# Performance work log

Hardware: AMD Instinct MI355X
Metric: run time of the kernel (lower is better)

Reference implementation:

```python
import jax, jax.numpy as jnp
import numpy as np

D_MODEL = 5120
NUM_HEADS = 128
HEAD_DIM = D_MODEL // NUM_HEADS  # 40
LATENT = 1536


def setup_inputs() -> dict:
    key = jax.random.key(0)
    ks = jax.random.split(key, 9)
    B, S = 2, 1024
    scale = 0.02
    return {
        "x": jax.random.normal(ks[0], (B, S, D_MODEL), dtype=jnp.float32),
        "Wq": jax.random.normal(ks[1], (D_MODEL, D_MODEL), dtype=jnp.float32) * scale,
        "bq": jnp.zeros((D_MODEL,), dtype=jnp.float32),
        "Wc": jax.random.normal(ks[2], (D_MODEL, LATENT), dtype=jnp.float32) * scale,
        "bc": jnp.zeros((LATENT,), dtype=jnp.float32),
        "Wk": jax.random.normal(ks[3], (LATENT, D_MODEL), dtype=jnp.float32) * scale,
        "bk": jnp.zeros((D_MODEL,), dtype=jnp.float32),
        "Wv": jax.random.normal(ks[4], (LATENT, D_MODEL), dtype=jnp.float32) * scale,
        "bv": jnp.zeros((D_MODEL,), dtype=jnp.float32),
    }


def reference(x, Wq, bq, Wc, bc, Wk, bk, Wv, bv):
    B, S, _ = x.shape
    H, Dh = NUM_HEADS, HEAD_DIM
    # projections
    q = x @ Wq + bq                     # [B,S,D]
    kv_latent = x @ Wc + bc             # [B,S,L]
    k = kv_latent @ Wk + bk             # [B,S,D]
    v = kv_latent @ Wv + bv             # [B,S,D]
    # split heads -> [B,H,S,Dh]
    q = q.reshape(B, S, H, Dh).transpose(0, 2, 1, 3)
    k = k.reshape(B, S, H, Dh).transpose(0, 2, 1, 3)
    v = v.reshape(B, S, H, Dh).transpose(0, 2, 1, 3)
    scores = jnp.einsum("bhqd,bhkd->bhqk", q, k) / jnp.sqrt(jnp.float32(Dh))
    attn = jax.nn.softmax(scores, axis=-1)
    out = jnp.einsum("bhqk,bhkd->bhqd", attn, v)  # [B,H,S,Dh]
    return out.transpose(0, 2, 1, 3).reshape(B, S, H * Dh)
```

## Files before the change

### kernel.cpp

```cpp
#include <hip/hip_runtime.h>
#include <hip/hip_bf16.h>

typedef __attribute__((ext_vector_type(8))) __bf16 bf16x8;
typedef __attribute__((ext_vector_type(4))) __bf16 bf16x4;
typedef __attribute__((ext_vector_type(4))) float f32x4;

#define MFMA16(a, b, c) __builtin_amdgcn_mfma_f32_16x16x32_bf16((a), (b), (c), 0, 0, 0)

#if __has_builtin(__builtin_amdgcn_exp2f)
#define EXP2F(x) __builtin_amdgcn_exp2f(x)
#else
#define EXP2F(x) exp2f(x)
#endif

#define GLDS16(g, l)                                                             \
    __builtin_amdgcn_global_load_lds((const __attribute__((address_space(1))) void*)(g), \
                                     (__attribute__((address_space(3))) void*)(l), 16, 0, 0)

#define BARRIER()                          \
    do {                                   \
        asm volatile("" ::: "memory");     \
        __builtin_amdgcn_s_barrier();      \
        asm volatile("" ::: "memory");     \
    } while (0)

#define WAIT_LGKM0() asm volatile("s_waitcnt lgkmcnt(0)" ::: "memory")
#define VM6 asm volatile("s_waitcnt vmcnt(6)" ::: "memory")
#define VM8 asm volatile("s_waitcnt vmcnt(8)" ::: "memory")
#define VM0 asm volatile("s_waitcnt vmcnt(0)" ::: "memory")
#define VMNONE ((void)0)
#define KEEP(x) x
#define DROP(x)

static __device__ __forceinline__ unsigned short cvt_bf(float f) {
    return __builtin_bit_cast(unsigned short, (__bf16)f);
}

static __device__ __forceinline__ bf16x8 bf8_zero() {
    uint4 z = make_uint4(0, 0, 0, 0);
    return __builtin_bit_cast(bf16x8, z);
}

__global__ __launch_bounds__(256) void xconv(const float* __restrict__ X,
                                             unsigned short* __restrict__ Xb, int n) {
    int i = (blockIdx.x * 256 + threadIdx.x) * 4;
    if (i < n) {
        float4 f = *(const float4*)(X + i);
        ushort4 o;
        o.x = cvt_bf(f.x); o.y = cvt_bf(f.y); o.z = cvt_bf(f.z); o.w = cvt_bf(f.w);
        *(ushort4*)(Xb + i) = o;
    }
}

__global__ __launch_bounds__(256) void wconv(const float* __restrict__ W,
                                             unsigned short* __restrict__ WT, int K, int N) {
    __shared__ unsigned short tile[32][33];
    int n0 = blockIdx.x * 32, k0 = blockIdx.y * 32;
    int c = threadIdx.x & 31, r8 = threadIdx.x >> 5;
#pragma unroll
    for (int it = 0; it < 4; ++it) {
        int r = r8 + it * 8;
        tile[r][c] = cvt_bf(W[(size_t)(k0 + r) * N + n0 + c]);
    }
    __syncthreads();
    int k2 = (threadIdx.x & 15) * 2, n8 = threadIdx.x >> 4;
#pragma unroll
    for (int it = 0; it < 2; ++it) {
        int n = n8 + it * 16;
        ushort2 o;
        o.x = tile[k2][n];
        o.y = tile[k2 + 1][n];
        *(ushort2*)&WT[(size_t)(n0 + n) * K + k0 + k2] = o;
    }
}


#define STAGE_A(S, H, KT)                                                              \
    do {                                                                               \
        GLDS16(aS[H][0] + (size_t)(KT) * 64, &Abuf[S][(H) * 8192 + wid * 512]);        \
        GLDS16(aS[H][1] + (size_t)(KT) * 64, &Abuf[S][(H) * 8192 + 4096 + wid * 512]); \
    } while (0)
#define STAGE_B(S, H, KT)                                                              \
    do {                                                                               \
        GLDS16(bS[H][0] + (size_t)(KT) * 64, &Bbuf[S][(H) * 8192 + wid * 512]);        \
        GLDS16(bS[H][1] + (size_t)(KT) * 64, &Bbuf[S][(H) * 8192 + 4096 + wid * 512]); \
    } while (0)

#define LDA_HALF(S, QM)                                                                   \
    do {                                                                                  \
        _Pragma("unroll") for (int mi = 0; mi < 4; ++mi)                                  \
            _Pragma("unroll") for (int kh = 0; kh < 2; ++kh)                              \
                af[mi][kh] =                                                              \
                    *(const bf16x8*)&Abuf[S][((QM) * 8192 + aoff + mi * 1024) ^ (kh * 32)]; \
    } while (0)
#define LDB_HALF(S, QN, BF)                                                               \
    do {                                                                                  \
        _Pragma("unroll") for (int ni = 0; ni < 2; ++ni)                                  \
            _Pragma("unroll") for (int kh = 0; kh < 2; ++kh)                              \
                BF[ni][kh] =                                                              \
                    *(const bf16x8*)&Bbuf[S][((QN) * 8192 + boff + ni * 1024) ^ (kh * 32)]; \
    } while (0)

#define MMAQ(QM, QN, BF)                                                                \
    do {                                                                                \
        _Pragma("unroll") for (int mi = 0; mi < 4; ++mi)                                \
            _Pragma("unroll") for (int ni = 0; ni < 2; ++ni)                            \
                _Pragma("unroll") for (int kh = 0; kh < 2; ++kh)                        \
                    acc[(QM) * 4 + mi][(QN) * 2 + ni] =                                 \
                        MFMA16(af[mi][kh], BF[ni][kh], acc[(QM) * 4 + mi][(QN) * 2 + ni]); \
    } while (0)

#define KTILE_V2(S, T, STG1, STG2, VMOP, RDNEXT)       \
    {                                                  \
        const int s_ = (S);                            \
        LDB_HALF(s_, 1, bf1);                          \
        STG1(STAGE_B(s_ ^ 1, 0, (T) + 1);)             \
        __builtin_amdgcn_s_setprio(1);                 \
        MMAQ(0, 0, bf0);                               \
        __builtin_amdgcn_s_setprio(0);                 \
        WAIT_LGKM0();                                  \
        BARRIER();                                     \
        STG2(STAGE_A(s_, 0, (T) + 2);                  \
             STAGE_B(s_, 1, (T) + 2);)                 \
        __builtin_amdgcn_s_setprio(1);                 \
        MMAQ(0, 1, bf1);                               \
        __builtin_amdgcn_s_setprio(0);                 \
        LDA_HALF(s_, 1);                               \
        __builtin_amdgcn_s_setprio(1);                 \
        MMAQ(1, 1, bf1);                               \
        __builtin_amdgcn_s_setprio(0);                 \
        WAIT_LGKM0();                                  \
        BARRIER();                                     \
        STG2(STAGE_A(s_, 1, (T) + 2);)                 \
        __builtin_amdgcn_s_setprio(1);                 \
        MMAQ(1, 0, bf0);                               \
        __builtin_amdgcn_s_setprio(0);                 \
        VMOP;                                          \
        BARRIER();                                     \
        RDNEXT(LDA_HALF(s_ ^ 1, 0); LDB_HALF(s_ ^ 1, 0, bf0);) \
    }

__global__ __launch_bounds__(512, 2) void gemm256(const unsigned short* __restrict__ A, int lda,
                                                  const unsigned short* __restrict__ BT, int ldb,
                                                  const float* __restrict__ bias0,
                                                  const float* __restrict__ bias1, int nsplit,
                                                  unsigned short* __restrict__ C, int ldc,
                                                  int K, float s0, float s1, int gx) {
    __shared__ __align__(16) unsigned short Abuf[2][16384];
    __shared__ __align__(16) unsigned short Bbuf[2][16384];

    int nwg = gridDim.x, orig = blockIdx.x;
    int cpx = nwg >> 3;
    int wgid = (orig & 7) * cpx + (orig >> 3);
    int tm = wgid / gx, tn = wgid % gx;
    int m0 = tm * 256, n0 = tn * 256;

    int tid = threadIdx.x, lane = tid & 63, wid = tid >> 6;
    int wm = wid >> 2, wn = wid & 3;
    int lrow = lane & 15, lkg = lane >> 4;

    int t5 = tid >> 3;
    int cole = ((tid & 7) ^ ((tid >> 3) & 7)) << 3;
    const unsigned short* aS[2][2];
    const unsigned short* bS[2][2];
#pragma unroll
    for (int H = 0; H < 2; ++H)
#pragma unroll
        for (int c = 0; c < 2; ++c) {
            int rA = (c << 7) | (H << 6) | t5;
            int rB = (((c << 1) | (t5 >> 5)) << 6) | (H << 5) | (t5 & 31);
            aS[H][c] = A + (size_t)(m0 + rA) * lda + cole;
            bS[H][c] = BT + (size_t)(n0 + rB) * ldb + cole;
        }

    int xorc = (lkg * 8) ^ ((lrow & 7) << 3);
    int aoff = wm * 4096 + lrow * 64 + xorc;
    int boff = wn * 2048 + lrow * 64 + xorc;

    f32x4 acc[8][4];
#pragma unroll
    for (int i = 0; i < 8; ++i)
#pragma unroll
        for (int j = 0; j < 4; ++j) acc[i][j] = (f32x4){0.f, 0.f, 0.f, 0.f};
    bf16x8 af[4][2], bf0[2][2], bf1[2][2];

    const int nkt = K >> 6;

    STAGE_A(0, 0, 0); STAGE_A(0, 1, 0); STAGE_B(0, 0, 0); STAGE_B(0, 1, 0);
    STAGE_A(1, 0, 1); STAGE_B(1, 1, 1); STAGE_A(1, 1, 1);
    VM6;
    BARRIER();
    LDA_HALF(0, 0);
    LDB_HALF(0, 0, bf0);

    int t = 0;
    for (; t + 2 < nkt; ++t) KTILE_V2(t & 1, t, KEEP, KEEP, VM6, KEEP);
    KTILE_V2(t & 1, t, KEEP, DROP, VM0, KEEP);
    ++t;
    KTILE_V2(t & 1, t, DROP, DROP, VMNONE, DROP);

#pragma unroll
    for (int ni = 0; ni < 4; ++ni) {
        int col = n0 + wn * 64 + ni * 16 + lrow;
        float bval = (col < nsplit) ? bias0[col] : bias1[col - nsplit];
        float scl = (col < nsplit) ? s0 : s1;
#pragma unroll
        for (int mi = 0; mi < 8; ++mi) {
            int row = m0 + wm * 128 + mi * 16 + lkg * 4;
#pragma unroll
            for (int j = 0; j < 4; ++j)
                C[(size_t)(row + j) * ldc + col] = cvt_bf((acc[mi][ni][j] + bval) * scl);
        }
    }
}

#define STG128(S, KT)                                                                  \
    do {                                                                               \
        _Pragma("unroll") for (int i_ = 0; i_ < 4; ++i_)                               \
            GLDS16(Ag + (size_t)(i_ * 32) * lda + (size_t)(KT) * 64,                   \
                   &Abuf[S][i_ * 2048 + wid * 512]);                                   \
        _Pragma("unroll") for (int i_ = 0; i_ < 4; ++i_)                               \
            GLDS16(Bg + (size_t)(i_ * 32) * ldb + (size_t)(KT) * 64,                   \
                   &Bbuf[S][i_ * 2048 + wid * 512]);                                   \
    } while (0)

__global__ __launch_bounds__(256, 2) void gemm128(const unsigned short* __restrict__ A, int lda,
                                                  const unsigned short* __restrict__ BT, int ldb,
                                                  const float* __restrict__ bias0,
                                                  const float* __restrict__ bias1, int nsplit,
                                                  unsigned short* __restrict__ C, int ldc,
                                                  int K, float s0, float s1, int gy) {
    __shared__ __align__(16) unsigned short Abuf[2][8192];
    __shared__ __align__(16) unsigned short Bbuf[2][8192];

    int b = blockIdx.x;
    int tm = b % gy, tn = b / gy;
    int m0 = tm * 128, n0 = tn * 128;
    int tid = threadIdx.x, lane = tid & 63, wid = tid >> 6;
    int wm = wid >> 1, wn = wid & 1;
    int lrow = lane & 15, lkg = lane >> 4;

    int srow = tid >> 3;
    int cole = ((tid & 7) ^ ((tid >> 3) & 7)) << 3;
    const unsigned short* Ag = A + (size_t)(m0 + srow) * lda + cole;
    const unsigned short* Bg = BT + (size_t)(n0 + srow) * ldb + cole;

    int xorc8 = (lrow & 7) << 3;
    int aoff = (wm * 64 + lrow) * 64;
    int boff = (wn * 64 + lrow) * 64;

    f32x4 acc[4][4];
#pragma unroll
    for (int i = 0; i < 4; ++i)
#pragma unroll
        for (int j = 0; j < 4; ++j) acc[i][j] = (f32x4){0.f, 0.f, 0.f, 0.f};

    const int nkt = K >> 6;
    STG128(0, 0);
    for (int t = 0; t < nkt; ++t) {
        const int cur = t & 1;
        if (t + 1 < nkt) {
            STG128(cur ^ 1, t + 1);
            VM8;
        } else {
            VM0;
        }
        BARRIER();
        bf16x8 af[4][2], bv[4][2];
#pragma unroll
        for (int mi = 0; mi < 4; ++mi)
#pragma unroll
            for (int kh = 0; kh < 2; ++kh)
                af[mi][kh] = *(const bf16x8*)&Abuf[cur][aoff + mi * 1024 + (((kh * 4 + lkg) << 3) ^ xorc8)];
#pragma unroll
        for (int ni = 0; ni < 4; ++ni)
#pragma unroll
            for (int kh = 0; kh < 2; ++kh)
                bv[ni][kh] = *(const bf16x8*)&Bbuf[cur][boff + ni * 1024 + (((kh * 4 + lkg) << 3) ^ xorc8)];
        __builtin_amdgcn_s_setprio(1);
#pragma unroll
        for (int mi = 0; mi < 4; ++mi)
#pragma unroll
            for (int ni = 0; ni < 4; ++ni)
#pragma unroll
                for (int kh = 0; kh < 2; ++kh)
                    acc[mi][ni] = MFMA16(af[mi][kh], bv[ni][kh], acc[mi][ni]);
        __builtin_amdgcn_s_setprio(0);
        BARRIER();
    }

#pragma unroll
    for (int ni = 0; ni < 4; ++ni) {
        int col = n0 + wn * 64 + ni * 16 + lrow;
        float bval = (col < nsplit) ? bias0[col] : bias1[col - nsplit];
        float scl = (col < nsplit) ? s0 : s1;
#pragma unroll
        for (int mi = 0; mi < 4; ++mi) {
            int row = m0 + wm * 64 + mi * 16 + lkg * 4;
#pragma unroll
            for (int j = 0; j < 4; ++j)
                C[(size_t)(row + j) * ldc + col] = cvt_bf((acc[mi][ni][j] + bval) * scl);
        }
    }
}

__global__ __launch_bounds__(256) void attn(const unsigned short* __restrict__ q, int ldq,
                                            const unsigned short* __restrict__ k, int ldk,
                                            const unsigned short* __restrict__ v, int ldv,
                                            float* __restrict__ out) {
    const int S = 1024, D = 5120, Dh = 40;
    int b = blockIdx.z, h = blockIdx.y, qt = blockIdx.x;
    int t = threadIdx.x, lane = t & 63, wid = t >> 6;
    int lrow = lane & 15, lkg = lane >> 4;

    __shared__ __align__(16) unsigned short Ks[64 * 72];
    __shared__ __align__(16) unsigned short Vs[64 * 72];
    __shared__ __align__(16) unsigned short Ps[4][16 * 72];

    const size_t qbase = ((size_t)b * S) * ldq + (size_t)h * Dh;
    const size_t kbase = ((size_t)b * S) * ldk + (size_t)h * Dh;
    const size_t vbase = ((size_t)b * S) * ldv + (size_t)h * Dh;
    int q0 = qt * 64 + wid * 16;

    bf16x8 qf0, qf1;
    {
        const unsigned short* qp = q + qbase + (size_t)(q0 + lrow) * ldq;
        qf0 = *(const bf16x8*)(qp + lkg * 8);
        qf1 = (lkg == 0) ? *(const bf16x8*)(qp + 32) : bf8_zero();
    }

    f32x4 acc[3];
#pragma unroll
    for (int nb = 0; nb < 3; ++nb) acc[nb] = (f32x4){0.f, 0.f, 0.f, 0.f};
    float mrun = -INFINITY, lrun = 0.f;

    for (int kt = 0; kt < 16; ++kt) {
        __syncthreads();
#pragma unroll
        for (int it = 0; it < 2; ++it) {
            int idx = t + it * 256;
            int rr = idx >> 3, cc = idx & 7;
            uint4 val = make_uint4(0, 0, 0, 0);
            if (cc < 5) val = *(const uint4*)(k + kbase + (size_t)(kt * 64 + rr) * ldk + cc * 8);
            *(uint4*)&Ks[rr * 72 + cc * 8] = val;
        }
#pragma unroll
        for (int it = 0; it < 2; ++it) {
            int idx = t + it * 256;
            int rr = idx & 63, cc = idx >> 6;
            if (cc < 6) {
                uint4 val = make_uint4(0, 0, 0, 0);
                if (cc < 5) val = *(const uint4*)(v + vbase + (size_t)(kt * 64 + rr) * ldv + cc * 8);
                const unsigned short* pv = (const unsigned short*)&val;
#pragma unroll
                for (int j = 0; j < 8; ++j) Vs[(cc * 8 + j) * 72 + rr] = pv[j];
            }
        }
        __syncthreads();

        f32x4 sf[4];
#pragma unroll
        for (int nb = 0; nb < 4; ++nb) {
            sf[nb] = (f32x4){0.f, 0.f, 0.f, 0.f};
            bf16x8 kf0 = *(const bf16x8*)&Ks[(nb * 16 + lrow) * 72 + lkg * 8];
            bf16x8 kf1 = *(const bf16x8*)&Ks[(nb * 16 + lrow) * 72 + 32 + lkg * 8];
            sf[nb] = MFMA16(kf0, qf0, sf[nb]);
            sf[nb] = MFMA16(kf1, qf1, sf[nb]);
        }

        float tm = sf[0][0];
#pragma unroll
        for (int nb = 0; nb < 4; ++nb)
#pragma unroll
            for (int i = 0; i < 4; ++i) tm = fmaxf(tm, sf[nb][i]);
        tm = fmaxf(tm, __shfl_xor(tm, 16));
        tm = fmaxf(tm, __shfl_xor(tm, 32));

        float mn = mrun, al = 1.0f;
        bool resc = !__all(tm <= mrun + 11.0f);
        if (resc) {
            mn = fmaxf(mrun, tm);
            al = EXP2F(mrun - mn);
            mrun = mn;
        }
        float rs = 0.f;
#pragma unroll
        for (int nb = 0; nb < 4; ++nb) {
            bf16x4 pk;
#pragma unroll
            for (int i = 0; i < 4; ++i) {
                float p = EXP2F(sf[nb][i] - mn);
                rs += p;
                pk[i] = (__bf16)p;
            }
            *(bf16x4*)&Ps[wid][lrow * 72 + nb * 16 + lkg * 4] = pk;
        }
        rs += __shfl_xor(rs, 16);
        rs += __shfl_xor(rs, 32);
        lrun = lrun * al + rs;

        if (resc) {
            float alr[4];
#pragma unroll
            for (int i = 0; i < 4; ++i) alr[i] = __shfl(al, lkg * 4 + i);
#pragma unroll
            for (int nb = 0; nb < 3; ++nb)
#pragma unroll
                for (int i = 0; i < 4; ++i) acc[nb][i] *= alr[i];
        }

#pragma unroll
        for (int kk = 0; kk < 2; ++kk) {
            bf16x8 pf = *(const bf16x8*)&Ps[wid][lrow * 72 + kk * 32 + lkg * 8];
#pragma unroll
            for (int nb = 0; nb < 3; ++nb) {
                bf16x8 vf = *(const bf16x8*)&Vs[(nb * 16 + lrow) * 72 + kk * 32 + lkg * 8];
                acc[nb] = MFMA16(pf, vf, acc[nb]);
            }
        }
    }

    float lr[4];
#pragma unroll
    for (int i = 0; i < 4; ++i) lr[i] = __shfl(lrun, lkg * 4 + i);
#pragma unroll
    for (int i = 0; i < 4; ++i) {
        float inv = 1.0f / lr[i];
        int s = q0 + lkg * 4 + i;
#pragma unroll
        for (int nb = 0; nb < 3; ++nb) {
            int d = nb * 16 + lrow;
            if (d < Dh) out[((size_t)(b * S + s)) * D + h * Dh + d] = acc[nb][i] * inv;
        }
    }
}

extern "C" void kernel_launch(void* const* d_in, const int* in_sizes, int n_in,
                              void* d_out, int out_size, void* d_ws, size_t ws_size,
                              hipStream_t stream) {
    const int M = 2048, D = 5120, L = 1536, NQ = D + L , NKV = 2 * D ;
    const float* x  = (const float*)d_in[0];
    const float* Wq = (const float*)d_in[1];
    const float* bq = (const float*)d_in[2];
    const float* Wc = (const float*)d_in[3];
    const float* bc = (const float*)d_in[4];
    const float* Wk = (const float*)d_in[5];
    const float* bk = (const float*)d_in[6];
    const float* Wv = (const float*)d_in[7];
    const float* bv = (const float*)d_in[8];
    float* out = (float*)d_out;

    unsigned short* ws = (unsigned short*)d_ws;
    size_t off = 0;
    unsigned short* xb    = ws + off; off += (size_t)M * D;
    unsigned short* WqcT  = ws + off; off += (size_t)NQ * D;
    unsigned short* WkvT  = ws + off; off += (size_t)NKV * L;
    unsigned short* qkvb  = ws + off; off += (size_t)M * NQ;
    unsigned short* kvout = ws + off; off += (size_t)M * NKV;

    xconv<<<(M * D) / 1024, 256, 0, stream>>>(x, xb, M * D);
    wconv<<<dim3(D / 32, D / 32), 256, 0, stream>>>(Wq, WqcT, D, D);
    wconv<<<dim3(L / 32, D / 32), 256, 0, stream>>>(Wc, WqcT + (size_t)D * D, D, L);
    wconv<<<dim3(D / 32, L / 32), 256, 0, stream>>>(Wk, WkvT, L, D);
    wconv<<<dim3(D / 32, L / 32), 256, 0, stream>>>(Wv, WkvT + (size_t)D * L, L, D);

    const float qscale = 1.4426950408889634f / 6.324555320336759f;

    gemm256<<<dim3((NQ / 256) * (M / 256)), 512, 0, stream>>>(xb, D, WqcT, D, bq, bc, D,
                                                              qkvb, NQ, D, qscale, 1.0f,
                                                              NQ / 256);
    gemm128<<<dim3((NKV / 128) * (M / 128)), 256, 0, stream>>>(qkvb + D, NQ, WkvT, L, bk, bv, D,
                                                               kvout, NKV, L, 1.0f, 1.0f,
                                                               M / 128);

    attn<<<dim3(1024 / 64, 128, 2), 256, 0, stream>>>(qkvb, NQ, kvout, NKV, kvout + D, NKV, out);
}
```

Before: 490.2 us.

## Prefetch next K/V tile into registers, merge weight conversions into one launch

The attention kernel now loads the next 64-row K/V tile from global memory into registers right after the LDS barrier, so the loads overlap the current tile's MFMA and softmax work. It also raises wave priority around the MFMA sections. The four weight-transpose launches become a single kernel that dispatches on block index, cutting launch overhead and tail gaps. The prefetch costs extra registers, which may reduce occupancy.

```diff
diff --git a/kernel.cpp b/kernel.cpp
--- a/kernel.cpp
+++ b/kernel.cpp
@@ -52,10 +52,25 @@
     }
 }
 
-__global__ __launch_bounds__(256) void wconv(const float* __restrict__ W,
-                                             unsigned short* __restrict__ WT, int K, int N) {
+__global__ __launch_bounds__(256) void wconv4(const float* __restrict__ Wq,
+                                              const float* __restrict__ Wc,
+                                              const float* __restrict__ Wk,
+                                              const float* __restrict__ Wv,
+                                              unsigned short* __restrict__ dqc,
+                                              unsigned short* __restrict__ dkv) {
+    const int D = 5120, L = 1536;
+    int b = blockIdx.x;
+    const float* W;
+    unsigned short* WT;
+    int K, N;
+    if (b < 25600) { W = Wq; WT = dqc; K = D; N = D; }
+    else if (b < 33280) { b -= 25600; W = Wc; WT = dqc + (size_t)D * D; K = D; N = L; }
+    else if (b < 40960) { b -= 33280; W = Wk; WT = dkv; K = L; N = D; }
+    else { b -= 40960; W = Wv; WT = dkv + (size_t)D * L; K = L; N = D; }
+    int nx = N / 32;
+    int n0 = (b % nx) * 32, k0 = (b / nx) * 32;
+
     __shared__ unsigned short tile[32][33];
-    int n0 = blockIdx.x * 32, k0 = blockIdx.y * 32;
     int c = threadIdx.x & 31, r8 = threadIdx.x >> 5;
 #pragma unroll
     for (int it = 0; it < 4; ++it) {
@@ -73,7 +88,6 @@
         *(ushort2*)&WT[(size_t)(n0 + n) * K + k0 + k2] = o;
     }
 }
-
 
 #define STAGE_A(S, H, KT)                                                              \
     do {                                                                               \
@@ -318,8 +332,6 @@
     __shared__ __align__(16) unsigned short Ps[4][16 * 72];
 
     const size_t qbase = ((size_t)b * S) * ldq + (size_t)h * Dh;
-    const size_t kbase = ((size_t)b * S) * ldk + (size_t)h * Dh;
-    const size_t vbase = ((size_t)b * S) * ldv + (size_t)h * Dh;
     int q0 = qt * 64 + wid * 16;
 
     bf16x8 qf0, qf1;
@@ -329,6 +341,21 @@
         qf1 = (lkg == 0) ? *(const bf16x8*)(qp + 32) : bf8_zero();
     }
 
+    int rrK = t >> 3, ccK = t & 7;
+    int rrV = t & 63, ccV = t >> 6;
+    const unsigned short* kp = k + ((size_t)b * S) * ldk + (size_t)h * Dh +
+                               (size_t)rrK * ldk + ccK * 8;
+    const unsigned short* vp = v + ((size_t)b * S) * ldv + (size_t)h * Dh +
+                               (size_t)rrV * ldv + ccV * 8;
+    const size_t kstep = (size_t)64 * ldk, vstep = (size_t)64 * ldv;
+
+    uint4 kv0, kv1, vv0, vv1;
+    kv0 = kv1 = vv0 = vv1 = make_uint4(0, 0, 0, 0);
+    if (ccK < 5) { kv0 = *(const uint4*)kp; kv1 = *(const uint4*)(kp + 32 * ldk); }
+    vv0 = *(const uint4*)vp;
+    if (ccV == 0) vv1 = *(const uint4*)(vp + 32);
+    kp += kstep; vp += vstep;
+
     f32x4 acc[3];
 #pragma unroll
     for (int nb = 0; nb < 3; ++nb) acc[nb] = (f32x4){0.f, 0.f, 0.f, 0.f};
@@ -336,29 +363,31 @@
 
     for (int kt = 0; kt < 16; ++kt) {
         __syncthreads();
-#pragma unroll
-        for (int it = 0; it < 2; ++it) {
-            int idx = t + it * 256;
-            int rr = idx >> 3, cc = idx & 7;
-            uint4 val = make_uint4(0, 0, 0, 0);
-            if (cc < 5) val = *(const uint4*)(k + kbase + (size_t)(kt * 64 + rr) * ldk + cc * 8);
-            *(uint4*)&Ks[rr * 72 + cc * 8] = val;
-        }
-#pragma unroll
-        for (int it = 0; it < 2; ++it) {
-            int idx = t + it * 256;
-            int rr = idx & 63, cc = idx >> 6;
-            if (cc < 6) {
-                uint4 val = make_uint4(0, 0, 0, 0);
-                if (cc < 5) val = *(const uint4*)(v + vbase + (size_t)(kt * 64 + rr) * ldv + cc * 8);
-                const unsigned short* pv = (const unsigned short*)&val;
-#pragma unroll
-                for (int j = 0; j < 8; ++j) Vs[(cc * 8 + j) * 72 + rr] = pv[j];
+        uint4 w0 = (ccK < 5) ? kv0 : make_uint4(0, 0, 0, 0);
+        uint4 w1 = (ccK < 5) ? kv1 : make_uint4(0, 0, 0, 0);
+        *(uint4*)&Ks[rrK * 72 + ccK * 8] = w0;
+        *(uint4*)&Ks[(rrK + 32) * 72 + ccK * 8] = w1;
+        {
+            const unsigned short* pv = (const unsigned short*)&vv0;
+#pragma unroll
+            for (int j = 0; j < 8; ++j) Vs[(ccV * 8 + j) * 72 + rrV] = pv[j];
+            if (ccV < 2) {
+                uint4 z = (ccV == 0) ? vv1 : make_uint4(0, 0, 0, 0);
+                const unsigned short* pz = (const unsigned short*)&z;
+#pragma unroll
+                for (int j = 0; j < 8; ++j) Vs[((ccV + 4) * 8 + j) * 72 + rrV] = pz[j];
             }
         }
         __syncthreads();
+        if (kt + 1 < 16) {
+            if (ccK < 5) { kv0 = *(const uint4*)kp; kv1 = *(const uint4*)(kp + 32 * ldk); }
+            vv0 = *(const uint4*)vp;
+            if (ccV == 0) vv1 = *(const uint4*)(vp + 32);
+            kp += kstep; vp += vstep;
+        }
 
         f32x4 sf[4];
+        __builtin_amdgcn_s_setprio(1);
 #pragma unroll
         for (int nb = 0; nb < 4; ++nb) {
             sf[nb] = (f32x4){0.f, 0.f, 0.f, 0.f};
@@ -367,6 +396,7 @@
             sf[nb] = MFMA16(kf0, qf0, sf[nb]);
             sf[nb] = MFMA16(kf1, qf1, sf[nb]);
         }
+        __builtin_amdgcn_s_setprio(0);
 
         float tm = sf[0][0];
 #pragma unroll
@@ -409,6 +439,7 @@
                 for (int i = 0; i < 4; ++i) acc[nb][i] *= alr[i];
         }
 
+        __builtin_amdgcn_s_setprio(1);
 #pragma unroll
         for (int kk = 0; kk < 2; ++kk) {
             bf16x8 pf = *(const bf16x8*)&Ps[wid][lrow * 72 + kk * 32 + lkg * 8];
@@ -418,6 +449,7 @@
                 acc[nb] = MFMA16(pf, vf, acc[nb]);
             }
         }
+        __builtin_amdgcn_s_setprio(0);
     }
 
     float lr[4];
@@ -459,10 +491,7 @@
     unsigned short* kvout = ws + off; off += (size_t)M * NKV;
 
     xconv<<<(M * D) / 1024, 256, 0, stream>>>(x, xb, M * D);
-    wconv<<<dim3(D / 32, D / 32), 256, 0, stream>>>(Wq, WqcT, D, D);
-    wconv<<<dim3(L / 32, D / 32), 256, 0, stream>>>(Wc, WqcT + (size_t)D * D, D, L);
-    wconv<<<dim3(D / 32, L / 32), 256, 0, stream>>>(Wk, WkvT, L, D);
-    wconv<<<dim3(D / 32, L / 32), 256, 0, stream>>>(Wv, WkvT + (size_t)D * L, L, D);
+    wconv4<<<48640, 256, 0, stream>>>(Wq, Wc, Wk, Wv, WqcT, WkvT);
 
     const float qscale = 1.4426950408889634f / 6.324555320336759f;
 
```

Measured after the change: 470.7 us. 4.0% less time.
